# Kernel tuning notes

Hardware: AMD Instinct MI355X
Metric: run time of the kernel (lower is better)

Reference implementation:

```python
import jax, jax.numpy as jnp
import numpy as np

N_NODES = 100000
N_EDGES = 3200000
IN_DIM = 512
HID_DIM = 16
OUT_DIM = 64


def _gcn_layer(E, X, W, b, n_nodes):
    # Standard GCN layer (CatGNN GCNLayer_MPNN_2):
    # add self-loops, symmetric deg^-1/2 normalization, project, gather-scatter sum.
    src = jnp.concatenate([E[0], jnp.arange(n_nodes, dtype=E.dtype)])
    dst = jnp.concatenate([E[1], jnp.arange(n_nodes, dtype=E.dtype)])
    deg = jax.ops.segment_sum(jnp.ones_like(dst, dtype=X.dtype), dst, num_segments=n_nodes)
    dinv = jnp.where(deg > 0, jax.lax.rsqrt(deg), 0.0)  # deg^-1/2, safe
    h = X @ W  # [N, d_out] project BEFORE aggregation (cheaper gather)
    norm = dinv[src] * dinv[dst]  # [E+N]
    msg = h[src] * norm[:, None]  # gather + scale
    out = jax.ops.segment_sum(msg, dst, num_segments=n_nodes)  # scatter-sum
    return out + b


def setup_inputs() -> dict:
    key = jax.random.key(0)
    k1, k2, k3, k4, k5 = jax.random.split(key, 5)
    V = jnp.arange(N_NODES, dtype=jnp.int64)
    E = jax.random.randint(k1, (2, N_EDGES), 0, N_NODES, dtype=jnp.int64)
    X = jax.random.normal(k2, (N_NODES, IN_DIM), dtype=jnp.float32)
    # Glorot-style init for layer weights
    W1 = jax.random.normal(k3, (IN_DIM, HID_DIM), dtype=jnp.float32) / np.sqrt(IN_DIM)
    b1 = jnp.zeros((HID_DIM,), dtype=jnp.float32)
    W2 = jax.random.normal(k4, (HID_DIM, OUT_DIM), dtype=jnp.float32) / np.sqrt(HID_DIM)
    b2 = jnp.zeros((OUT_DIM,), dtype=jnp.float32)
    return {"V": V, "E": E, "X": X, "W1": W1, "b1": b1, "W2": W2, "b2": b2}


def reference(V, E, X, W1, b1, W2, b2):
    n_nodes = V.shape[0]
    H = jax.nn.relu(_gcn_layer(E, X, W1, b1, n_nodes))
    # dropout is identity in eval mode
    H = _gcn_layer(E, H, W2, b2, n_nodes)
    return H
```

## Files before the change

### kernel.cpp

```cpp
#include <hip/hip_runtime.h>

#define HID 16
#define ODIM 64
#define IDIM 512
#define BKB 8
#define BKS 256
#define PTILE 8192
#define PITER 16
#define PAD 16

__device__ __forceinline__ int wave_scan_block(int v, int t, int* wsum) {
    int lane = t & 63, w = t >> 6;
    int x = v;
#pragma unroll
    for (int off = 1; off < 64; off <<= 1) {
        int y = __shfl_up(x, off, 64);
        if (lane >= off) x += y;
    }
    if (lane == 63) wsum[w] = x;
    __syncthreads();
    if (w == 0) {
        int s = (lane < 8) ? wsum[lane] : 0;
#pragma unroll
        for (int off = 1; off < 8; off <<= 1) {
            int y = __shfl_up(s, off, 64);
            if (lane >= off) s += y;
        }
        if (lane < 8) wsum[lane] = s;
    }
    __syncthreads();
    return x + (w ? wsum[w - 1] : 0);
}

__global__ __launch_bounds__(512) void k_bhist(const int* __restrict__ dst,
                                               int* __restrict__ bcnt, int ne, int nbk) {
    __shared__ int h[512];
    int t = threadIdx.x;
    h[t] = 0;
    __syncthreads();
    int stride = gridDim.x * 512;
    for (int e = blockIdx.x * 512 + t; e < ne; e += stride)
        atomicAdd(&h[dst[e] >> BKB], 1);
    __syncthreads();
    if (t < nbk && h[t]) atomicAdd(&bcnt[t * PAD], h[t]);
}

__global__ __launch_bounds__(512) void k_bscan(const int* __restrict__ bcnt,
                                               int* __restrict__ bbase,
                                               int* __restrict__ bcur, int nbk) {
    __shared__ int wsum[8];
    int t = threadIdx.x;
    int v = (t < nbk) ? bcnt[t * PAD] : 0;
    int inc = wave_scan_block(v, t, wsum);
    if (t < nbk) { int b = inc - v; bbase[t] = b; bcur[t * PAD] = b; }
}

__global__ __launch_bounds__(512) void k_part(const int* __restrict__ src,
                                              const int* __restrict__ dst,
                                              int* __restrict__ bcur,
                                              unsigned int* __restrict__ ebuf, int ne) {
    __shared__ int h[512], sc[512], base[512], lcur[512], wsum[8];
    __shared__ unsigned int sval[PTILE];
    __shared__ int saddr[PTILE];
    int e0 = blockIdx.x * PTILE;
    int m = ne - e0; if (m > PTILE) m = PTILE;
    int t = threadIdx.x;
    h[t] = 0;
    __syncthreads();
    int dv[PITER];
#pragma unroll
    for (int it = 0; it < PITER; ++it) {
        int k = t + it * 512;
        int d = 0;
        if (k < m) { d = dst[e0 + k]; atomicAdd(&h[d >> BKB], 1); }
        dv[it] = d;
    }
    __syncthreads();
    int hv = h[t];
    int inc = wave_scan_block(hv, t, wsum);
    sc[t] = inc;
    base[t] = hv ? atomicAdd(&bcur[t * PAD], hv) : 0;
    lcur[t] = 0;
    __syncthreads();
#pragma unroll
    for (int it = 0; it < PITER; ++it) {
        int k = t + it * 512;
        if (k < m) {
            int d = dv[it];
            int b = d >> BKB;
            int r = atomicAdd(&lcur[b], 1);
            int slot = sc[b] - h[b] + r;
            sval[slot] = ((unsigned int)src[e0 + k] << BKB) | (unsigned int)(d & (BKS - 1));
            saddr[slot] = base[b] + r;
        }
    }
    __syncthreads();
#pragma unroll
    for (int it = 0; it < PITER; ++it) {
        int k = t + it * 512;
        if (k < m) ebuf[saddr[k]] = sval[k];
    }
}

__global__ __launch_bounds__(512) void k_csr(const int* __restrict__ bbase,
                                             const int* __restrict__ bcnt,
                                             const unsigned int* __restrict__ ebuf,
                                             int* __restrict__ cnt,
                                             int* __restrict__ row_start,
                                             int* __restrict__ csr_src, int n) {
    __shared__ int h[256], sc[256], lc[256], wsum[8];
    int bk = blockIdx.x;
    int node0 = bk << BKB;
    int ebase = bbase[bk];
    int ecnt = bcnt[bk * PAD];
    int t = threadIdx.x;
    if (t < 256) { h[t] = 0; lc[t] = 0; }
    __syncthreads();
    for (int k = t; k < ecnt; k += 512) atomicAdd(&h[ebuf[ebase + k] & (BKS - 1)], 1);
    __syncthreads();
    int hv = (t < 256) ? h[t] : 0;
    int inc = wave_scan_block(hv, t, wsum);
    if (t < 256) {
        sc[t] = inc;
        int node = node0 + t;
        if (node < n) { cnt[node] = hv; row_start[node] = ebase + inc - hv; }
    }
    __syncthreads();
    for (int k = t; k < ecnt; k += 512) {
        unsigned int p = ebuf[ebase + k];
        int dl = p & (BKS - 1);
        int r = atomicAdd(&lc[dl], 1);
        csr_src[ebase + sc[dl] - h[dl] + r] = (int)(p >> BKB);
    }
}

__device__ __forceinline__ void fmaq(float4& a, float s, float4 w) {
    a.x = fmaf(s, w.x, a.x);
    a.y = fmaf(s, w.y, a.y);
    a.z = fmaf(s, w.z, a.z);
    a.w = fmaf(s, w.w, a.w);
}

__global__ __launch_bounds__(256) void k_proj1(const float* __restrict__ X,
                                               const float* __restrict__ W1,
                                               const int* __restrict__ cnt,
                                               float* __restrict__ hs1, int n) {
    int i = blockIdx.x * 256 + threadIdx.x;
    if (i >= n) return;

    const float4* __restrict__ xr = (const float4*)(X + (size_t)i * IDIM);
    const float4* __restrict__ W4 = (const float4*)W1;
    float4 a0 = make_float4(0.f, 0.f, 0.f, 0.f), a1 = a0, a2 = a0, a3 = a0;

#pragma unroll 4
    for (int k4 = 0; k4 < IDIM / 4; ++k4) {
        float4 x = xr[k4];
        const float4* w = W4 + k4 * 16;
        fmaq(a0, x.x, w[0]);  fmaq(a1, x.x, w[1]);  fmaq(a2, x.x, w[2]);  fmaq(a3, x.x, w[3]);
        fmaq(a0, x.y, w[4]);  fmaq(a1, x.y, w[5]);  fmaq(a2, x.y, w[6]);  fmaq(a3, x.y, w[7]);
        fmaq(a0, x.z, w[8]);  fmaq(a1, x.z, w[9]);  fmaq(a2, x.z, w[10]); fmaq(a3, x.z, w[11]);
        fmaq(a0, x.w, w[12]); fmaq(a1, x.w, w[13]); fmaq(a2, x.w, w[14]); fmaq(a3, x.w, w[15]);
    }

    float di = rsqrtf((float)(cnt[i] + 1));
    a0.x *= di; a0.y *= di; a0.z *= di; a0.w *= di;
    a1.x *= di; a1.y *= di; a1.z *= di; a1.w *= di;
    a2.x *= di; a2.y *= di; a2.z *= di; a2.w *= di;
    a3.x *= di; a3.y *= di; a3.z *= di; a3.w *= di;
    float4* h4 = (float4*)(hs1 + (size_t)i * HID);
    h4[0] = a0; h4[1] = a1; h4[2] = a2; h4[3] = a3;
}

__device__ __forceinline__ void acc4(float4& a, float4 v) {
    a.x += v.x; a.y += v.y; a.z += v.z; a.w += v.w;
}

__device__ __forceinline__ float4 gacc(int rs, int c, int q,
                                       const int* __restrict__ csr_src,
                                       const float4* __restrict__ h4,
                                       float4 acc) {
    float4 accB = make_float4(0.f, 0.f, 0.f, 0.f);
    float4 accC = accB, accD = accB;
    int k = 0;
    int head = (-rs) & 3;
    if (head > c) head = c;
    for (; k < head; ++k)
        acc4(acc, h4[(size_t)csr_src[rs + k] * 4 + q]);
    for (; k + 15 < c; k += 16) {
        int4 s0 = *(const int4*)(csr_src + rs + k);
        int4 s1 = *(const int4*)(csr_src + rs + k + 4);
        int4 s2 = *(const int4*)(csr_src + rs + k + 8);
        int4 s3 = *(const int4*)(csr_src + rs + k + 12);
        float4 v0 = h4[(size_t)s0.x * 4 + q];
        float4 v1 = h4[(size_t)s0.y * 4 + q];
        float4 v2 = h4[(size_t)s0.z * 4 + q];
        float4 v3 = h4[(size_t)s0.w * 4 + q];
        float4 v4 = h4[(size_t)s1.x * 4 + q];
        float4 v5 = h4[(size_t)s1.y * 4 + q];
        float4 v6 = h4[(size_t)s1.z * 4 + q];
        float4 v7 = h4[(size_t)s1.w * 4 + q];
        float4 v8 = h4[(size_t)s2.x * 4 + q];
        float4 v9 = h4[(size_t)s2.y * 4 + q];
        float4 va = h4[(size_t)s2.z * 4 + q];
        float4 vb = h4[(size_t)s2.w * 4 + q];
        float4 vc = h4[(size_t)s3.x * 4 + q];
        float4 vd = h4[(size_t)s3.y * 4 + q];
        float4 ve = h4[(size_t)s3.z * 4 + q];
        float4 vf = h4[(size_t)s3.w * 4 + q];
        acc4(acc, v0);  acc4(accB, v4);  acc4(accC, v8);  acc4(accD, vc);
        acc4(acc, v1);  acc4(accB, v5);  acc4(accC, v9);  acc4(accD, vd);
        acc4(acc, v2);  acc4(accB, v6);  acc4(accC, va);  acc4(accD, ve);
        acc4(acc, v3);  acc4(accB, v7);  acc4(accC, vb);  acc4(accD, vf);
    }
    for (; k + 3 < c; k += 4) {
        int4 s = *(const int4*)(csr_src + rs + k);
        acc4(acc, h4[(size_t)s.x * 4 + q]);
        acc4(accB, h4[(size_t)s.y * 4 + q]);
        acc4(accC, h4[(size_t)s.z * 4 + q]);
        acc4(accD, h4[(size_t)s.w * 4 + q]);
    }
    for (; k < c; ++k)
        acc4(acc, h4[(size_t)csr_src[rs + k] * 4 + q]);
    acc4(accB, accC);
    acc4(acc, accD);
    acc4(acc, accB);
    return acc;
}

__global__ __launch_bounds__(256) void k_gather_mid(const int* __restrict__ row_start,
                                                    const int* __restrict__ cnt,
                                                    const int* __restrict__ csr_src,
                                                    const float* __restrict__ hs,
                                                    const float* __restrict__ b1,
                                                    float* __restrict__ outbuf, int n) {
    int tid = blockIdx.x * blockDim.x + threadIdx.x;
    int i = tid >> 2;
    int q = tid & 3;
    if (i >= n) return;
    const float4* h4 = (const float4*)hs;
    int rs = row_start[i];
    int c = cnt[i];
    float4 acc = gacc(rs, c, q, csr_src, h4, h4[(size_t)i * 4 + q]);
    float di = rsqrtf((float)(c + 1));
    float4 b = ((const float4*)b1)[q];
    float4 r;
    r.x = fmaxf(fmaf(di, acc.x, b.x), 0.f) * di;
    r.y = fmaxf(fmaf(di, acc.y, b.y), 0.f) * di;
    r.z = fmaxf(fmaf(di, acc.z, b.z), 0.f) * di;
    r.w = fmaxf(fmaf(di, acc.w, b.w), 0.f) * di;
    ((float4*)outbuf)[(size_t)i * 4 + q] = r;
}

__global__ __launch_bounds__(256) void k_gather(const int* __restrict__ row_start,
                                                const int* __restrict__ cnt,
                                                const int* __restrict__ csr_src,
                                                const float* __restrict__ hs,
                                                float* __restrict__ agg, int n) {
    int tid = blockIdx.x * blockDim.x + threadIdx.x;
    int i = tid >> 2;
    int q = tid & 3;
    if (i >= n) return;
    const float4* h4 = (const float4*)hs;
    int rs = row_start[i];
    int c = cnt[i];
    float4 acc = gacc(rs, c, q, csr_src, h4, h4[(size_t)i * 4 + q]);
    ((float4*)agg)[(size_t)i * 4 + q] = acc;
}

__global__ __launch_bounds__(256) void k_out(const int* __restrict__ cnt,
                                             const float* __restrict__ agg2,
                                             const float* __restrict__ W2,
                                             const float* __restrict__ b2,
                                             float* __restrict__ out, int n) {
    __shared__ float Ws[HID * ODIM];
    __shared__ float bs[ODIM];
    int t = threadIdx.x;
    for (int u = t; u < HID * ODIM; u += 256) Ws[u] = W2[u];
    if (t < ODIM) bs[t] = b2[t];
    __syncthreads();

    int j = t & 63;
    int slot = t >> 6;
    int i0 = blockIdx.x * 16 + slot * 4;

    float wc[HID];
#pragma unroll
    for (int k = 0; k < HID; ++k) wc[k] = Ws[k * ODIM + j];
    float bj = bs[j];

    const float4* g4 = (const float4*)agg2;
#pragma unroll
    for (int u = 0; u < 4; ++u) {
        int i = i0 + u;
        if (i < n) {
            float4 g0 = g4[(size_t)i * 4 + 0];
            float4 g1 = g4[(size_t)i * 4 + 1];
            float4 g2 = g4[(size_t)i * 4 + 2];
            float4 g3 = g4[(size_t)i * 4 + 3];
            float acc = g0.x * wc[0]  + g0.y * wc[1]  + g0.z * wc[2]  + g0.w * wc[3]
                      + g1.x * wc[4]  + g1.y * wc[5]  + g1.z * wc[6]  + g1.w * wc[7]
                      + g2.x * wc[8]  + g2.y * wc[9]  + g2.z * wc[10] + g2.w * wc[11]
                      + g3.x * wc[12] + g3.y * wc[13] + g3.z * wc[14] + g3.w * wc[15];
            float di = rsqrtf((float)(cnt[i] + 1));
            out[(size_t)i * ODIM + j] = fmaf(di, acc, bj);
        }
    }
}

extern "C" void kernel_launch(void* const* d_in, const int* in_sizes, int n_in,
                              void* d_out, int out_size, void* d_ws, size_t ws_size,
                              hipStream_t stream) {
    const int* E = (const int*)d_in[1];
    const float* X = (const float*)d_in[2];
    const float* W1 = (const float*)d_in[3];
    const float* b1 = (const float*)d_in[4];
    const float* W2 = (const float*)d_in[5];
    const float* b2 = (const float*)d_in[6];
    float* out = (float*)d_out;

    const int n = in_sizes[0];
    const int ne = in_sizes[1] / 2;
    const int* src = E;
    const int* dst = E + ne;
    const int nbk = (n + BKS - 1) >> BKB;

    char* ws = (char*)d_ws;
    int* bcnt = (int*)ws;
    int* bbase = (int*)(ws + (32u << 10));
    int* bcur = (int*)(ws + (64u << 10));
    int* cnt = (int*)(ws + (1u << 20));
    int* row_start = (int*)(ws + (2u << 20));
    unsigned int* ebuf = (unsigned int*)(ws + (3u << 20));
    float* B1 = (float*)(ws + (3u << 20));
    float* B2 = (float*)(ws + (10u << 20));
    int* csr_src = (int*)(ws + (17u << 20));

    hipMemsetAsync(bcnt, 0, nbk * PAD * sizeof(int), stream);
    k_bhist<<<256, 512, 0, stream>>>(dst, bcnt, ne, nbk);
    k_bscan<<<1, 512, 0, stream>>>(bcnt, bbase, bcur, nbk);
    k_part<<<(ne + PTILE - 1) / PTILE, 512, 0, stream>>>(src, dst, bcur, ebuf, ne);
    k_csr<<<nbk, 512, 0, stream>>>(bbase, bcnt, ebuf, cnt, row_start, csr_src, n);

    k_proj1<<<(n + 255) / 256, 256, 0, stream>>>(X, W1, cnt, B1, n);
    k_gather_mid<<<(n * 4 + 255) / 256, 256, 0, stream>>>(row_start, cnt, csr_src, B1, b1, B2, n);
    k_gather<<<(n * 4 + 255) / 256, 256, 0, stream>>>(row_start, cnt, csr_src, B2, B1, n);
    k_out<<<(n + 15) / 16, 256, 0, stream>>>(cnt, B1, W2, b2, out, n);
}
```

Measured before the change: 497.3 us.

## Sort nodes by degree via counting-sort permutation to balance gather waves

Result: slower. 754.4 us (+51.7%).

```diff
diff --git a/kernel.cpp b/kernel.cpp
--- a/kernel.cpp
+++ b/kernel.cpp
@@ -107,7 +107,8 @@
                                              const unsigned int* __restrict__ ebuf,
                                              int* __restrict__ cnt,
                                              int* __restrict__ row_start,
-                                             int* __restrict__ csr_src, int n) {
+                                             int* __restrict__ csr_src,
+                                             int* __restrict__ dh, int n) {
     __shared__ int h[256], sc[256], lc[256], wsum[8];
     int bk = blockIdx.x;
     int node0 = bk << BKB;
@@ -123,7 +124,12 @@
     if (t < 256) {
         sc[t] = inc;
         int node = node0 + t;
-        if (node < n) { cnt[node] = hv; row_start[node] = ebase + inc - hv; }
+        if (node < n) {
+            cnt[node] = hv;
+            row_start[node] = ebase + inc - hv;
+            int d = hv < 255 ? hv : 255;
+            atomicAdd(&dh[d * PAD], 1);
+        }
     }
     __syncthreads();
     for (int k = t; k < ecnt; k += 512) {
@@ -132,6 +138,32 @@
         int r = atomicAdd(&lc[dl], 1);
         csr_src[ebase + sc[dl] - h[dl] + r] = (int)(p >> BKB);
     }
+}
+
+__global__ __launch_bounds__(256) void k_dscan(const int* __restrict__ dh,
+                                               int* __restrict__ dcur) {
+    __shared__ int s[256];
+    int t = threadIdx.x;
+    int v = dh[t * PAD];
+    s[t] = v;
+    __syncthreads();
+    for (int off = 1; off < 256; off <<= 1) {
+        int u = (t >= off) ? s[t - off] : 0;
+        __syncthreads();
+        s[t] += u;
+        __syncthreads();
+    }
+    dcur[t * PAD] = s[t] - v;
+}
+
+__global__ __launch_bounds__(256) void k_dperm(const int* __restrict__ cnt,
+                                               int* __restrict__ dcur,
+                                               int* __restrict__ perm, int n) {
+    int i = blockIdx.x * 256 + threadIdx.x;
+    if (i >= n) return;
+    int d = cnt[i]; if (d > 255) d = 255;
+    int p = atomicAdd(&dcur[d * PAD], 1);
+    perm[p] = i;
 }
 
 __device__ __forceinline__ void fmaq(float4& a, float s, float4 w) {
@@ -230,13 +262,15 @@
 __global__ __launch_bounds__(256) void k_gather_mid(const int* __restrict__ row_start,
                                                     const int* __restrict__ cnt,
                                                     const int* __restrict__ csr_src,
+                                                    const int* __restrict__ perm,
                                                     const float* __restrict__ hs,
                                                     const float* __restrict__ b1,
                                                     float* __restrict__ outbuf, int n) {
     int tid = blockIdx.x * blockDim.x + threadIdx.x;
-    int i = tid >> 2;
+    int slot = tid >> 2;
     int q = tid & 3;
-    if (i >= n) return;
+    if (slot >= n) return;
+    int i = perm[slot];
     const float4* h4 = (const float4*)hs;
     int rs = row_start[i];
     int c = cnt[i];
@@ -254,12 +288,14 @@
 __global__ __launch_bounds__(256) void k_gather(const int* __restrict__ row_start,
                                                 const int* __restrict__ cnt,
                                                 const int* __restrict__ csr_src,
+                                                const int* __restrict__ perm,
                                                 const float* __restrict__ hs,
                                                 float* __restrict__ agg, int n) {
     int tid = blockIdx.x * blockDim.x + threadIdx.x;
-    int i = tid >> 2;
+    int slot = tid >> 2;
     int q = tid & 3;
-    if (i >= n) return;
+    if (slot >= n) return;
+    int i = perm[slot];
     const float4* h4 = (const float4*)hs;
     int rs = row_start[i];
     int c = cnt[i];
@@ -326,23 +362,28 @@
 
     char* ws = (char*)d_ws;
     int* bcnt = (int*)ws;
-    int* bbase = (int*)(ws + (32u << 10));
+    int* dh = (int*)(ws + (28u << 10));
+    int* bbase = (int*)(ws + (48u << 10));
     int* bcur = (int*)(ws + (64u << 10));
+    int* dcur = (int*)(ws + (128u << 10));
     int* cnt = (int*)(ws + (1u << 20));
     int* row_start = (int*)(ws + (2u << 20));
+    int* perm = (int*)(ws + (2u << 20) + (512u << 10));
     unsigned int* ebuf = (unsigned int*)(ws + (3u << 20));
     float* B1 = (float*)(ws + (3u << 20));
     float* B2 = (float*)(ws + (10u << 20));
     int* csr_src = (int*)(ws + (17u << 20));
 
-    hipMemsetAsync(bcnt, 0, nbk * PAD * sizeof(int), stream);
+    hipMemsetAsync(ws, 0, 44u << 10, stream);
     k_bhist<<<256, 512, 0, stream>>>(dst, bcnt, ne, nbk);
     k_bscan<<<1, 512, 0, stream>>>(bcnt, bbase, bcur, nbk);
     k_part<<<(ne + PTILE - 1) / PTILE, 512, 0, stream>>>(src, dst, bcur, ebuf, ne);
-    k_csr<<<nbk, 512, 0, stream>>>(bbase, bcnt, ebuf, cnt, row_start, csr_src, n);
+    k_csr<<<nbk, 512, 0, stream>>>(bbase, bcnt, ebuf, cnt, row_start, csr_src, dh, n);
+    k_dscan<<<1, 256, 0, stream>>>(dh, dcur);
+    k_dperm<<<(n + 255) / 256, 256, 0, stream>>>(cnt, dcur, perm, n);
 
     k_proj1<<<(n + 255) / 256, 256, 0, stream>>>(X, W1, cnt, B1, n);
-    k_gather_mid<<<(n * 4 + 255) / 256, 256, 0, stream>>>(row_start, cnt, csr_src, B1, b1, B2, n);
-    k_gather<<<(n * 4 + 255) / 256, 256, 0, stream>>>(row_start, cnt, csr_src, B2, B1, n);
+    k_gather_mid<<<(n * 4 + 255) / 256, 256, 0, stream>>>(row_start, cnt, csr_src, perm, B1, b1, B2, n);
+    k_gather<<<(n * 4 + 255) / 256, 256, 0, stream>>>(row_start, cnt, csr_src, perm, B2, B1, n);
     k_out<<<(n + 15) / 16, 256, 0, stream>>>(cnt, B1, W2, b2, out, n);
 }
```
